# Optimization experiments

Measured on AMD Instinct MI355X. Metric: run time of the kernel, lower is better.

Reference implementation:

```python
import jax, jax.numpy as jnp
from jax import lax
import numpy as np

BIG_I = jnp.int32(2 ** 30)   # background / +inf sentinel for labels
BIG_F = 1e6                  # +inf sentinel for distances (max true dist ~ H+W)


def cc_labels(fg):
    """8-connected component labeling via iterative min-label propagation.
    fg: (H, W) bool. Returns int32 labels; background pixels get BIG_I.
    Two pixels are in the same component iff their labels are equal
    (labels are min linear index of the component, which is all the loss uses)."""
    H, W = fg.shape
    lab0 = jnp.where(fg, jnp.arange(H * W, dtype=jnp.int32).reshape(H, W), BIG_I)

    def neigh_min(lab):
        p = jnp.pad(lab, 1, constant_values=BIG_I)
        m = lab
        for di in (-1, 0, 1):
            for dj in (-1, 0, 1):
                m = jnp.minimum(m, lax.dynamic_slice(p, (1 + di, 1 + dj), (H, W)))
        return jnp.where(fg, m, BIG_I)

    def body(state):
        lab, _ = state
        new = neigh_min(lab)
        return new, jnp.all(new == lab)

    lab, _ = lax.while_loop(lambda s: ~s[1], body, (lab0, jnp.array(False)))
    return lab


def _dt_axis(d, axis):
    # exact 1D L1 (min-plus, slope 1) lower envelope via forward/backward scans
    d = jnp.moveaxis(d, axis, 0)
    init = jnp.full(d.shape[1:], BIG_F, dtype=d.dtype)
    step = lambda c, x: ((jnp.minimum(x, c + 1.0),) * 2)
    _, fwd = lax.scan(step, init, d)
    _, bwd = lax.scan(step, init, d[::-1])
    return jnp.moveaxis(jnp.minimum(fwd, bwd[::-1]), 0, axis)


def l1_distance_transform(zero_mask):
    """Exact L1 distance to the nearest True pixel of zero_mask
    (== cv2.distanceTransform(DIST_L1, maskSize=3) on a binary image whose
    zero set is zero_mask). L1 DT is separable -> two 1D passes."""
    d0 = jnp.where(zero_mask, 0.0, BIG_F).astype(jnp.float32)
    return _dt_axis(_dt_axis(d0, 0), 1)


def _loss_one(result, pts):
    WEIGHT, GAP_W, CLUST_W = 100.0, 10.0, 90.0
    r0 = result[pts[0, 0], pts[0, 1]]
    r1 = result[pts[1, 0], pts[1, 1]]
    soa_inv = jnp.sum(1.0 - result)  # soa_cells_inv (per-pixel loop in original)
    fallback = (2.0 - (r0 + r1)) * WEIGHT
    loss_start = fallback

    img = lax.stop_gradient(jnp.round(result))  # result.round().detach()
    fg = img > 0.5
    lab = cc_labels(fg)
    sl = lab[pts[0, 0], pts[0, 1]]
    el = lab[pts[1, 0], pts[1, 1]]
    both = fg[pts[0, 0], pts[0, 1]] & fg[pts[1, 0], pts[1, 1]]  # start/end labels != 0

    # start_cluster = pixels of the start component (same set when start==end)
    start_mask = fg & (lab == sl) & both
    # modified label image: end component -> 0, everything else nonzero
    end_zero = fg & (lab == el)
    dist = l1_distance_transform(end_zero)  # distance to end component
    min_d = jnp.minimum(dist[pts[0, 0], pts[0, 1]],
                        jnp.min(jnp.where(start_mask, dist, BIG_F)))

    gap_loss = jnp.where(both, min_d * soa_inv * GAP_W * soa_inv, fallback)
    cluster_cells = jnp.sum(jnp.where(start_mask, result, 0.0))
    cluster_pen = jnp.where(both, cluster_cells * CLUST_W, fallback)
    return loss_start, gap_loss, cluster_pen


def setup_inputs():
    key = jax.random.key(0)
    k1, k2 = jax.random.split(key)
    result_given = jax.random.uniform(k1, (4, 1, 512, 512), dtype=jnp.float32)
    points_given = jax.random.randint(k2, (4, 2, 2), 0, 512, dtype=jnp.int32)
    return {"result_given": result_given, "points_given": points_given}


def reference(result_given, points_given):
    # Original loop overwrites loss/gap_loss/cluster_size_penalty each batch
    # iteration -> returned tuple reflects only the last batch element.
    ls, gl, cp = jax.vmap(_loss_one)(result_given[:, 0], points_given)
    return ls[-1], gl[-1], cp[-1]
```

## Files before the change

kernel.cpp:

```cpp
#include <hip/hip_runtime.h>

#define H 512
#define W 512
#define NPIX (H * W)
#define BIG_I 1073741824
#define BIG_F 1.0e6f
#define INF30 1.0e30f

struct Scal {
  float soa;
  unsigned int min_bits;
  float cluster;
  int sl;
  int pad[4];
};

__device__ unsigned g_bar1, g_bar2, g_bar3, g_doneS, g_doneD;

__device__ __forceinline__ void gbar(unsigned* cnt, bool wait) {
  __syncthreads();
  if (threadIdx.x == 0) {
    __threadfence();
    unsigned old = atomicAdd(cnt, 1u);
    if (wait) {
      unsigned target = (old & ~255u) + 256u;
      while (__hip_atomic_load(cnt, __ATOMIC_RELAXED, __HIP_MEMORY_SCOPE_AGENT) < target)
        __builtin_amdgcn_s_sleep(1);
      __threadfence();
    }
  }
  __syncthreads();
}

__device__ __forceinline__ int rep(int* lab, int v) {
  int cur = lab[v];
  if (cur == v) return v;
  int prev = v, next;
  while (cur > (next = lab[cur])) { lab[prev] = next; prev = cur; cur = next; }
  return cur;
}
__device__ __forceinline__ void unite(int* lab, int a, int b) {
  int ra = rep(lab, a), rb = rep(lab, b);
  while (ra != rb) {
    if (ra < rb) { int t = ra; ra = rb; rb = t; }
    int old = atomicCAS(&lab[ra], ra, rb);
    if (old == ra) break;
    ra = rep(lab, old);
    rb = rep(lab, rb);
  }
}
__device__ __forceinline__ int root_ph(int* lab, int v) {
  int p = lab[v];
  if (p == v) return v;
  int gp = lab[p];
  while (p != gp) {
    lab[v] = gp;
    v = p; p = gp; gp = lab[p];
  }
  return p;
}
__device__ __forceinline__ int runstart(unsigned m, int c) {
  unsigned z = ~m & ((1u << c) - 1u);
  return z ? (32 - __clz((int)z)) : 0;
}

__global__ __launch_bounds__(256) void k_fused(
    const float* __restrict__ img, const int* __restrict__ pts,
    int* __restrict__ lab, int* __restrict__ lab2, float* __restrict__ dist,
    Scal* __restrict__ s, float* __restrict__ Asoa, float* __restrict__ out) {
  __shared__ union {
    struct { int uf[1024]; unsigned rmask[32]; float red[4]; } p1;
    struct { float laf[32][8]; float lbb[32][8]; float smin[4]; } p4;
  } sh;
  __shared__ int sflag;

  const int t = threadIdx.x;
  const int b = blockIdx.x;

  const int tileX = (b & 15) * 32;
  const int tileY = (b >> 4) * 32;
  const int r = t >> 3, c0 = (t & 7) * 4;
  const float4 x4 = *(const float4*)(img + (tileY + r) * W + tileX + c0);

  const int p0 = pts[0] * W + pts[1];
  const int p1x = pts[2] * W + pts[3];
  const float r0 = img[p0], r1 = img[p1x];
  const bool both = (rintf(r0) > 0.5f) && (rintf(r1) > 0.5f);
  const float fb = (2.0f - (r0 + r1)) * 100.0f;
  if (!both) {
    if (b == 0 && t == 0) { out[0] = fb; out[1] = fb; out[2] = fb; }
    return;
  }
  if (b == 0 && t == 0) {
    s->min_bits = __float_as_uint(BIG_F);
    s->cluster = 0.0f;
  }

  {
    float acc = 4.0f - (x4.x + x4.y + x4.z + x4.w);
    unsigned nib = (rintf(x4.x) > 0.5f ? 1u : 0u) | (rintf(x4.y) > 0.5f ? 2u : 0u)
                 | (rintf(x4.z) > 0.5f ? 4u : 0u) | (rintf(x4.w) > 0.5f ? 8u : 0u);
    unsigned m = nib << c0;
    m |= __shfl_xor(m, 1, 64);
    m |= __shfl_xor(m, 2, 64);
    m |= __shfl_xor(m, 4, 64);
    if ((t & 7) == 0) sh.p1.rmask[r] = m;
    unsigned startM = m & ~(m << 1);
    #pragma unroll
    for (int k = 0; k < 4; ++k) {
      int c = c0 + k;
      if ((startM >> c) & 1u) sh.p1.uf[(r << 5) + c] = (r << 5) + c;
    }
    __syncthreads();
    if (r > 0) {
      unsigned ma = sh.p1.rmask[r - 1];
      unsigned upM = m & ma & (~(m << 1) | ~(ma << 1));
      unsigned dL  = startM & (ma << 1) & ~ma;
      unsigned dR  = (m & ~(m >> 1)) & (ma >> 1) & ~ma;
      #pragma unroll
      for (int k = 0; k < 4; ++k) {
        int c = c0 + k;
        int myS = (r << 5) + runstart(m, c);
        if ((upM >> c) & 1u) unite(sh.p1.uf, myS, ((r - 1) << 5) + runstart(ma, c));
        if ((dL  >> c) & 1u) unite(sh.p1.uf, myS, ((r - 1) << 5) + runstart(ma, c - 1));
        if ((dR  >> c) & 1u) unite(sh.p1.uf, myS, ((r - 1) << 5) + c + 1);
      }
    }
    __syncthreads();
    int o[4];
    #pragma unroll
    for (int k = 0; k < 4; ++k) {
      int c = c0 + k;
      if ((m >> c) & 1u) {
        int rt = rep(sh.p1.uf, (r << 5) + runstart(m, c));
        o[k] = (tileY + (rt >> 5)) * W + tileX + (rt & 31);
      } else o[k] = BIG_I;
    }
    *(int4*)(lab + (tileY + r) * W + tileX + c0) = make_int4(o[0], o[1], o[2], o[3]);
    for (int off = 32; off; off >>= 1) acc += __shfl_down(acc, off, 64);
    if ((t & 63) == 0) sh.p1.red[t >> 6] = acc;
    __syncthreads();
    if (t == 0) Asoa[b] = sh.p1.red[0] + sh.p1.red[1] + sh.p1.red[2] + sh.p1.red[3];
  }
  gbar(&g_bar1, true);

  {
    int lane = t & 63;
    int gid = b * 256 + t;
    if (gid < 7680) {
      int bb = gid >> 9, j = gid & 511;
      int i = (bb + 1) * 32;
      int p = i * W + j, q = p - W;
      int a  = lab[p];
      int u0 = lab[q];
      int um = (j > 0)   ? lab[q - 1] : BIG_I;
      int up = (j < 511) ? lab[q + 1] : BIG_I;
      int a_prev = __shfl_up(a, 1, 64);
      if (lane == 0) a_prev = (j > 0) ? lab[p - 1] : BIG_I;
      if (a != BIG_I) {
        if (um != BIG_I && a != a_prev) unite(lab, a, um);
        if (u0 != BIG_I && u0 != um) unite(lab, a, u0);
        if (up != BIG_I && up != u0 && !(u0 == BIG_I && up == um)) unite(lab, a, up);
      }
    } else if (gid < 15360) {
      int t2 = gid - 7680;
      int bb = t2 >> 9, i = t2 & 511;
      int j = (bb + 1) * 32;
      int p = i * W + j;
      int lp = lab[p], ll = lab[p - 1];
      int lpp = __shfl_up(lp, 1, 64);
      int llp = __shfl_up(ll, 1, 64);
      if (lane == 0) {
        lpp = (i > 0) ? lab[p - W] : BIG_I;
        llp = (i > 0) ? lab[p - W - 1] : BIG_I;
      }
      bool fgp = lp != BIG_I, fgl = ll != BIG_I;
      if (fgp && fgl && !(lp == lpp && ll == llp)) unite(lab, lp, ll);
      if ((i & 31) && i > 0) {
        if (fgp && llp != BIG_I && lp != lpp) unite(lab, lp, llp);
        if (fgl && lpp != BIG_I && ll != llp) unite(lab, ll, lpp);
      }
    } else if (b == 60 && t < 64) {
      float a = Asoa[t] + Asoa[t + 64] + Asoa[t + 128] + Asoa[t + 192];
      for (int off = 32; off; off >>= 1) a += __shfl_down(a, off, 64);
      if (t == 0) s->soa = a;
    }
  }
  gbar(&g_bar2, true);

  if (t < 128) {
    int lane = t & 63;
    int row = b * 2 + (t >> 6);
    int el = -1, sl2 = -1;
    if (lane == 0) {
      el = root_ph(lab, lab[p1x]);
      sl2 = root_ph(lab, lab[p0]);
      if (t == 0) sflag = (el == sl2);
      if (b == 0 && t == 0) s->sl = sl2;
    }
    el = __shfl(el, 0, 64);
    sl2 = __shfl(sl2, 0, 64);
    const bool skip = (el == sl2);
    const int4* lp = (const int4*)(lab + row * W) + lane * 2;
    int4 a = lp[0], bq = lp[1];
    int v[8] = {a.x, a.y, a.z, a.w, bq.x, bq.y, bq.z, bq.w};
    int psrc = -1, proot = -1;
    #pragma unroll
    for (int k = 0; k < 8; ++k) {
      if (v[k] == BIG_I) continue;
      if (v[k] == psrc) { v[k] = proot; continue; }
      psrc = v[k];
      proot = root_ph(lab, v[k]);
      v[k] = proot;
    }
    if (!skip) {
      int4* l2 = (int4*)(lab2 + row * W) + lane * 2;
      l2[0] = make_int4(v[0], v[1], v[2], v[3]);
      l2[1] = make_int4(v[4], v[5], v[6], v[7]);
    }
    const float4* ip = (const float4*)(img + row * W) + lane * 2;
    float4 i0q = ip[0], i1q = ip[1];
    float cv = 0.0f;
    if (v[0] == sl2) cv += i0q.x;
    if (v[1] == sl2) cv += i0q.y;
    if (v[2] == sl2) cv += i0q.z;
    if (v[3] == sl2) cv += i0q.w;
    if (v[4] == sl2) cv += i1q.x;
    if (v[5] == sl2) cv += i1q.y;
    if (v[6] == sl2) cv += i1q.z;
    if (v[7] == sl2) cv += i1q.w;
    for (int off = 32; off; off >>= 1) cv += __shfl_down(cv, off, 64);
    if (lane == 0 && cv != 0.0f) atomicAdd(&s->cluster, cv);
    if (!skip) {
      float d[8];
      #pragma unroll
      for (int k = 0; k < 8; ++k) d[k] = (v[k] == el) ? 0.0f : BIG_F;
      int j0 = lane * 8;
      float pf[8], sb[8];
      float m = INF30;
      #pragma unroll
      for (int k = 0; k < 8; ++k) { m = fminf(m, d[k] - (float)(j0 + k)); pf[k] = m; }
      float tf = m;
      m = INF30;
      #pragma unroll
      for (int k = 7; k >= 0; --k) { m = fminf(m, d[k] + (float)(j0 + k)); sb[k] = m; }
      float tb = m;
      float vv = tf;
      #pragma unroll
      for (int off = 1; off < 64; off <<= 1) {
        float u = __shfl_up(vv, off, 64);
        if (lane >= off) vv = fminf(vv, u);
      }
      float ef = __shfl_up(vv, 1, 64); if (lane == 0) ef = INF30;
      vv = tb;
      #pragma unroll
      for (int off = 1; off < 64; off <<= 1) {
        float u = __shfl_down(vv, off, 64);
        if (lane < 64 - off) vv = fminf(vv, u);
      }
      float eb = __shfl_down(vv, 1, 64); if (lane == 63) eb = INF30;
      float o[8];
      #pragma unroll
      for (int k = 0; k < 8; ++k) {
        float j = (float)(j0 + k);
        o[k] = fminf(j + fminf(ef, pf[k]), -j + fminf(eb, sb[k]));
      }
      float4* dp = (float4*)(dist + row * W) + lane * 2;
      dp[0] = make_float4(o[0], o[1], o[2], o[3]);
      dp[1] = make_float4(o[4], o[5], o[6], o[7]);
    }
  }
  __syncthreads();
  const bool skipb = sflag != 0;

  if (skipb) {
    if (t == 0) {
      __threadfence();
      unsigned old = atomicAdd(&g_doneS, 1u);
      if ((old & 255u) == 255u) {
        out[0] = fb;
        out[1] = 0.0f;
        float cl = atomicAdd(&s->cluster, 0.0f);
        out[2] = cl * 90.0f;
      }
    }
    return;
  }

  if (b >= 64) { gbar(&g_bar3, false); return; }
  gbar(&g_bar3, true);

  {
    int sg = t >> 3, c = t & 7;
    int j = b * 8 + c;
    int i0 = sg * 16;
    float rr[16];
    float fa = INF30, fbk = INF30;
    #pragma unroll
    for (int il = 0; il < 16; ++il) {
      rr[il] = dist[(i0 + il) * W + j];
      float fi = (float)(i0 + il);
      fa = fminf(fa, rr[il] - fi);
      fbk = fminf(fbk, rr[il] + fi);
    }
    sh.p4.laf[sg][c] = fa;
    sh.p4.lbb[sg][c] = fbk;
    __syncthreads();
    float cf = INF30, cb = INF30;
    #pragma unroll
    for (int bb = 0; bb < 32; ++bb) {
      if (bb < sg) cf = fminf(cf, sh.p4.laf[bb][c]);
      if (bb > sg) cb = fminf(cb, sh.p4.lbb[bb][c]);
    }
    int slv = s->sl;
    float ff[16];
    float m = cf;
    #pragma unroll
    for (int il = 0; il < 16; ++il) {
      float fi = (float)(i0 + il);
      m = fminf(m, rr[il] - fi);
      ff[il] = fi + m;
    }
    m = cb;
    float dv = BIG_F;
    #pragma unroll
    for (int il = 15; il >= 0; --il) {
      int pix = (i0 + il) * W + j;
      float fi = (float)(i0 + il);
      m = fminf(m, rr[il] + fi);
      float o = fminf(ff[il], m - fi);
      if (lab2[pix] == slv) dv = fminf(dv, o);
      if (pix == p0) dv = fminf(dv, o);
    }
    for (int off = 32; off; off >>= 1)
      dv = fminf(dv, __shfl_down(dv, off, 64));
    if ((t & 63) == 0) sh.p4.smin[t >> 6] = dv;
    __syncthreads();
    if (t == 0) {
      float mm = fminf(fminf(sh.p4.smin[0], sh.p4.smin[1]),
                       fminf(sh.p4.smin[2], sh.p4.smin[3]));
      atomicMin(&s->min_bits, __float_as_uint(mm));
      __threadfence();
      unsigned old = atomicAdd(&g_doneD, 1u);
      if ((old & 63u) == 63u) {
        out[0] = fb;
        float min_d = __uint_as_float(atomicOr(&s->min_bits, 0u));
        float cl = atomicAdd(&s->cluster, 0.0f);
        float soa = s->soa;
        out[1] = min_d * soa * 10.0f * soa;
        out[2] = cl * 90.0f;
      }
    }
  }
}

extern "C" void kernel_launch(void* const* d_in, const int* in_sizes, int n_in,
                              void* d_out, int out_size, void* d_ws, size_t ws_size,
                              hipStream_t stream) {
  const float* img = (const float*)d_in[0] + 3 * NPIX;
  const int* pts = (const int*)d_in[1] + 3 * 4;
  float* out = (float*)d_out;

  int* lab = (int*)d_ws;
  float* dist = (float*)d_ws + NPIX;
  char* base = (char*)d_ws + (size_t)2 * NPIX * 4;
  Scal* s = (Scal*)base;
  float* Asoa = (float*)(base + 64);
  int* lab2 = (int*)(base + 64 + 1024);

  k_fused<<<256, 256, 0, stream>>>(img, pts, lab, lab2, dist, s, Asoa, out);
}
```

Before: 55.33 us.

## Replace global barrier before tile merge with neighbor flag waits

Each block now publishes a per-tile epoch flag and waits only for its adjacent tiles before merging its own boundary edges, instead of a grid-wide barrier followed by a grid-strided merge. Label finalization and cluster accumulation move into the tile's own registers, reusing the already-loaded pixels, and a separate barrier is added before the row distance pass, which now reads the finalized labels. The intent is to cut global barrier latency and redundant loads. In exchange it adds an epoch ticket, boundary-compressing find with relaxed atomics, and one more grid barrier on the non-skip path.

```diff
diff --git a/kernel.cpp b/kernel.cpp
--- a/kernel.cpp
+++ b/kernel.cpp
@@ -11,11 +11,12 @@
   float soa;
   unsigned int min_bits;
   float cluster;
-  int sl;
-  int pad[4];
+  int pad[5];
 };
 
-__device__ unsigned g_bar1, g_bar2, g_bar3, g_doneS, g_doneD;
+__device__ unsigned g_ticket;
+__device__ unsigned g_tileflag[256];
+__device__ unsigned g_barM, g_barR, g_barC, g_doneS, g_doneD;
 
 __device__ __forceinline__ void gbar(unsigned* cnt, bool wait) {
   __syncthreads();
@@ -59,6 +60,26 @@
   }
   return p;
 }
+__device__ __forceinline__ int lda(int* p) {
+  return __hip_atomic_load(p, __ATOMIC_RELAXED, __HIP_MEMORY_SCOPE_AGENT);
+}
+__device__ __forceinline__ int rep_bp(int* lab, int v) {
+  int cur = lda(&lab[v]);
+  if (cur == v) return v;
+  int prev = v, next;
+  while (cur > (next = lda(&lab[cur]))) { lab[prev] = next; prev = cur; cur = next; }
+  return cur;
+}
+__device__ __forceinline__ void unite_bp(int* lab, int a, int b) {
+  int ra = rep_bp(lab, a), rb = rep_bp(lab, b);
+  while (ra != rb) {
+    if (ra < rb) { int t = ra; ra = rb; rb = t; }
+    int old = atomicCAS(&lab[ra], ra, rb);
+    if (old == ra) break;
+    ra = rep_bp(lab, old);
+    rb = rep_bp(lab, rb);
+  }
+}
 __device__ __forceinline__ int runstart(unsigned m, int c) {
   unsigned z = ~m & ((1u << c) - 1u);
   return z ? (32 - __clz((int)z)) : 0;
@@ -72,13 +93,13 @@
     struct { int uf[1024]; unsigned rmask[32]; float red[4]; } p1;
     struct { float laf[32][8]; float lbb[32][8]; float smin[4]; } p4;
   } sh;
-  __shared__ int sflag;
+  __shared__ int s_sl, s_el, s_skip;
+  __shared__ float cred[4];
 
   const int t = threadIdx.x;
   const int b = blockIdx.x;
-
-  const int tileX = (b & 15) * 32;
-  const int tileY = (b >> 4) * 32;
+  const int tY = b >> 4, tX = b & 15;
+  const int tileX = tX * 32, tileY = tY * 32;
   const int r = t >> 3, c0 = (t & 7) * 4;
   const float4 x4 = *(const float4*)(img + (tileY + r) * W + tileX + c0);
 
@@ -91,11 +112,19 @@
     if (b == 0 && t == 0) { out[0] = fb; out[1] = fb; out[2] = fb; }
     return;
   }
+  unsigned ep1 = 0;
+  if (t < 64) {
+    unsigned tk = 0;
+    if (t == 0) tk = atomicAdd(&g_ticket, 1u);
+    tk = __shfl(tk, 0, 64);
+    ep1 = (tk >> 8) + 1u;
+  }
   if (b == 0 && t == 0) {
     s->min_bits = __float_as_uint(BIG_F);
     s->cluster = 0.0f;
   }
 
+  int o[4];
   {
     float acc = 4.0f - (x4.x + x4.y + x4.z + x4.w);
     unsigned nib = (rintf(x4.x) > 0.5f ? 1u : 0u) | (rintf(x4.y) > 0.5f ? 2u : 0u)
@@ -127,7 +156,6 @@
       }
     }
     __syncthreads();
-    int o[4];
     #pragma unroll
     for (int k = 0; k < 4; ++k) {
       int c = c0 + k;
@@ -140,144 +168,115 @@
     for (int off = 32; off; off >>= 1) acc += __shfl_down(acc, off, 64);
     if ((t & 63) == 0) sh.p1.red[t >> 6] = acc;
     __syncthreads();
-    if (t == 0) Asoa[b] = sh.p1.red[0] + sh.p1.red[1] + sh.p1.red[2] + sh.p1.red[3];
-  }
-  gbar(&g_bar1, true);
-
+    if (t == 0) {
+      Asoa[b] = sh.p1.red[0] + sh.p1.red[1] + sh.p1.red[2] + sh.p1.red[3];
+      __threadfence();
+      __hip_atomic_store(&g_tileflag[b], ep1, __ATOMIC_RELAXED,
+                         __HIP_MEMORY_SCOPE_AGENT);
+    }
+  }
+
+  if (t < 64) {
+    const bool hasH = tY < 15, hasV = tX < 15;
+    int nb = -1;
+    if (t == 0 && hasH)            nb = b + 16;
+    if (t == 1 && hasH && tX > 0)  nb = b + 15;
+    if (t == 2 && hasH && tX > 0)  nb = b - 1;
+    if (t == 3 && hasV)            nb = b + 1;
+    if (t == 4 && hasV && tY > 0)  nb = b - 16;
+    if (t == 5 && hasV && tY > 0)  nb = b - 15;
+    if (nb >= 0) {
+      while (__hip_atomic_load(&g_tileflag[nb], __ATOMIC_RELAXED,
+                               __HIP_MEMORY_SCOPE_AGENT) < ep1)
+        __builtin_amdgcn_s_sleep(1);
+    }
+    __threadfence();
+    if (t < 32) {
+      if (hasH) {
+        const int j = tileX + t;
+        const int p = (tileY + 32) * W + j, q = p - W;
+        int a  = lab[p];
+        int u0 = lab[q];
+        int um = (j > 0)   ? lab[q - 1] : BIG_I;
+        int up = (j < 511) ? lab[q + 1] : BIG_I;
+        int a_prev = __shfl_up(a, 1, 64);
+        if (t == 0) a_prev = (j > 0) ? lab[p - 1] : BIG_I;
+        if (a != BIG_I) {
+          if (um != BIG_I && a != a_prev) unite_bp(lab, a, um);
+          if (u0 != BIG_I && u0 != um) unite_bp(lab, a, u0);
+          if (up != BIG_I && up != u0 && !(u0 == BIG_I && up == um)) unite_bp(lab, a, up);
+        }
+      }
+    } else {
+      if (hasV) {
+        const int il = t - 32;
+        const int i = tileY + il;
+        const int p = i * W + tileX + 32;
+        int lp = lab[p], ll = lab[p - 1];
+        int lpp = __shfl_up(lp, 1, 64);
+        int llp = __shfl_up(ll, 1, 64);
+        if (il == 0) {
+          lpp = (i > 0) ? lab[p - W] : BIG_I;
+          llp = (i > 0) ? lab[p - W - 1] : BIG_I;
+        }
+        bool fgp = lp != BIG_I, fgl = ll != BIG_I;
+        if (fgp && fgl && !(lp == lpp && ll == llp)) unite_bp(lab, lp, ll);
+        if (il != 0) {
+          if (fgp && llp != BIG_I && lp != lpp) unite_bp(lab, lp, llp);
+          if (fgl && lpp != BIG_I && ll != llp) unite_bp(lab, ll, lpp);
+        }
+      }
+    }
+  }
+  gbar(&g_barM, true);
+
+  if (t == 0) {
+    int e  = root_ph(lab, lab[p1x]);
+    int s2 = root_ph(lab, lab[p0]);
+    s_el = e; s_sl = s2; s_skip = (e == s2);
+  }
+  if (b == 60 && t >= 64 && t < 128) {
+    int l = t & 63;
+    float a = Asoa[l] + Asoa[l + 64] + Asoa[l + 128] + Asoa[l + 192];
+    for (int off = 32; off; off >>= 1) a += __shfl_down(a, off, 64);
+    if (l == 0) s->soa = a;
+  }
+  int fin[4];
   {
-    int lane = t & 63;
-    int gid = b * 256 + t;
-    if (gid < 7680) {
-      int bb = gid >> 9, j = gid & 511;
-      int i = (bb + 1) * 32;
-      int p = i * W + j, q = p - W;
-      int a  = lab[p];
-      int u0 = lab[q];
-      int um = (j > 0)   ? lab[q - 1] : BIG_I;
-      int up = (j < 511) ? lab[q + 1] : BIG_I;
-      int a_prev = __shfl_up(a, 1, 64);
-      if (lane == 0) a_prev = (j > 0) ? lab[p - 1] : BIG_I;
-      if (a != BIG_I) {
-        if (um != BIG_I && a != a_prev) unite(lab, a, um);
-        if (u0 != BIG_I && u0 != um) unite(lab, a, u0);
-        if (up != BIG_I && up != u0 && !(u0 == BIG_I && up == um)) unite(lab, a, up);
-      }
-    } else if (gid < 15360) {
-      int t2 = gid - 7680;
-      int bb = t2 >> 9, i = t2 & 511;
-      int j = (bb + 1) * 32;
-      int p = i * W + j;
-      int lp = lab[p], ll = lab[p - 1];
-      int lpp = __shfl_up(lp, 1, 64);
-      int llp = __shfl_up(ll, 1, 64);
-      if (lane == 0) {
-        lpp = (i > 0) ? lab[p - W] : BIG_I;
-        llp = (i > 0) ? lab[p - W - 1] : BIG_I;
-      }
-      bool fgp = lp != BIG_I, fgl = ll != BIG_I;
-      if (fgp && fgl && !(lp == lpp && ll == llp)) unite(lab, lp, ll);
-      if ((i & 31) && i > 0) {
-        if (fgp && llp != BIG_I && lp != lpp) unite(lab, lp, llp);
-        if (fgl && lpp != BIG_I && ll != llp) unite(lab, ll, lpp);
-      }
-    } else if (b == 60 && t < 64) {
-      float a = Asoa[t] + Asoa[t + 64] + Asoa[t + 128] + Asoa[t + 192];
-      for (int off = 32; off; off >>= 1) a += __shfl_down(a, off, 64);
-      if (t == 0) s->soa = a;
-    }
-  }
-  gbar(&g_bar2, true);
-
-  if (t < 128) {
-    int lane = t & 63;
-    int row = b * 2 + (t >> 6);
-    int el = -1, sl2 = -1;
-    if (lane == 0) {
-      el = root_ph(lab, lab[p1x]);
-      sl2 = root_ph(lab, lab[p0]);
-      if (t == 0) sflag = (el == sl2);
-      if (b == 0 && t == 0) s->sl = sl2;
-    }
-    el = __shfl(el, 0, 64);
-    sl2 = __shfl(sl2, 0, 64);
-    const bool skip = (el == sl2);
-    const int4* lp = (const int4*)(lab + row * W) + lane * 2;
-    int4 a = lp[0], bq = lp[1];
-    int v[8] = {a.x, a.y, a.z, a.w, bq.x, bq.y, bq.z, bq.w};
     int psrc = -1, proot = -1;
     #pragma unroll
-    for (int k = 0; k < 8; ++k) {
-      if (v[k] == BIG_I) continue;
-      if (v[k] == psrc) { v[k] = proot; continue; }
-      psrc = v[k];
-      proot = root_ph(lab, v[k]);
-      v[k] = proot;
-    }
-    if (!skip) {
-      int4* l2 = (int4*)(lab2 + row * W) + lane * 2;
-      l2[0] = make_int4(v[0], v[1], v[2], v[3]);
-      l2[1] = make_int4(v[4], v[5], v[6], v[7]);
-    }
-    const float4* ip = (const float4*)(img + row * W) + lane * 2;
-    float4 i0q = ip[0], i1q = ip[1];
-    float cv = 0.0f;
-    if (v[0] == sl2) cv += i0q.x;
-    if (v[1] == sl2) cv += i0q.y;
-    if (v[2] == sl2) cv += i0q.z;
-    if (v[3] == sl2) cv += i0q.w;
-    if (v[4] == sl2) cv += i1q.x;
-    if (v[5] == sl2) cv += i1q.y;
-    if (v[6] == sl2) cv += i1q.z;
-    if (v[7] == sl2) cv += i1q.w;
-    for (int off = 32; off; off >>= 1) cv += __shfl_down(cv, off, 64);
-    if (lane == 0 && cv != 0.0f) atomicAdd(&s->cluster, cv);
-    if (!skip) {
-      float d[8];
-      #pragma unroll
-      for (int k = 0; k < 8; ++k) d[k] = (v[k] == el) ? 0.0f : BIG_F;
-      int j0 = lane * 8;
-      float pf[8], sb[8];
-      float m = INF30;
-      #pragma unroll
-      for (int k = 0; k < 8; ++k) { m = fminf(m, d[k] - (float)(j0 + k)); pf[k] = m; }
-      float tf = m;
-      m = INF30;
-      #pragma unroll
-      for (int k = 7; k >= 0; --k) { m = fminf(m, d[k] + (float)(j0 + k)); sb[k] = m; }
-      float tb = m;
-      float vv = tf;
-      #pragma unroll
-      for (int off = 1; off < 64; off <<= 1) {
-        float u = __shfl_up(vv, off, 64);
-        if (lane >= off) vv = fminf(vv, u);
-      }
-      float ef = __shfl_up(vv, 1, 64); if (lane == 0) ef = INF30;
-      vv = tb;
-      #pragma unroll
-      for (int off = 1; off < 64; off <<= 1) {
-        float u = __shfl_down(vv, off, 64);
-        if (lane < 64 - off) vv = fminf(vv, u);
-      }
-      float eb = __shfl_down(vv, 1, 64); if (lane == 63) eb = INF30;
-      float o[8];
-      #pragma unroll
-      for (int k = 0; k < 8; ++k) {
-        float j = (float)(j0 + k);
-        o[k] = fminf(j + fminf(ef, pf[k]), -j + fminf(eb, sb[k]));
-      }
-      float4* dp = (float4*)(dist + row * W) + lane * 2;
-      dp[0] = make_float4(o[0], o[1], o[2], o[3]);
-      dp[1] = make_float4(o[4], o[5], o[6], o[7]);
+    for (int k = 0; k < 4; ++k) {
+      if (o[k] == BIG_I) { fin[k] = BIG_I; continue; }
+      if (o[k] == psrc) { fin[k] = proot; continue; }
+      psrc = o[k];
+      proot = root_ph(lab, o[k]);
+      fin[k] = proot;
     }
   }
   __syncthreads();
-  const bool skipb = sflag != 0;
-
-  if (skipb) {
+  const int slv = s_sl, elv = s_el;
+  const bool skip = s_skip != 0;
+  float cv = 0.0f;
+  if (fin[0] == slv) cv += x4.x;
+  if (fin[1] == slv) cv += x4.y;
+  if (fin[2] == slv) cv += x4.z;
+  if (fin[3] == slv) cv += x4.w;
+  for (int off = 32; off; off >>= 1) cv += __shfl_down(cv, off, 64);
+  if ((t & 63) == 0) cred[t >> 6] = cv;
+  __syncthreads();
+  if (t == 0) {
+    float tot = cred[0] + cred[1] + cred[2] + cred[3];
+    if (tot != 0.0f) atomicAdd(&s->cluster, tot);
+  }
+  if (!skip)
+    *(int4*)(lab2 + (tileY + r) * W + tileX + c0) = make_int4(fin[0], fin[1], fin[2], fin[3]);
+
+  if (skip) {
     if (t == 0) {
       __threadfence();
       unsigned old = atomicAdd(&g_doneS, 1u);
       if ((old & 255u) == 255u) {
+        __threadfence();
         out[0] = fb;
         out[1] = 0.0f;
         float cl = atomicAdd(&s->cluster, 0.0f);
@@ -287,8 +286,52 @@
     return;
   }
 
-  if (b >= 64) { gbar(&g_bar3, false); return; }
-  gbar(&g_bar3, true);
+  gbar(&g_barR, true);
+  if (t < 128) {
+    int lane = t & 63;
+    int row = b * 2 + (t >> 6);
+    const int4* lp2 = (const int4*)(lab2 + row * W) + lane * 2;
+    int4 a = lp2[0], bq = lp2[1];
+    int v[8] = {a.x, a.y, a.z, a.w, bq.x, bq.y, bq.z, bq.w};
+    float d[8];
+    #pragma unroll
+    for (int k = 0; k < 8; ++k) d[k] = (v[k] == elv) ? 0.0f : BIG_F;
+    int j0 = lane * 8;
+    float pf[8], sb[8];
+    float m = INF30;
+    #pragma unroll
+    for (int k = 0; k < 8; ++k) { m = fminf(m, d[k] - (float)(j0 + k)); pf[k] = m; }
+    float tf = m;
+    m = INF30;
+    #pragma unroll
+    for (int k = 7; k >= 0; --k) { m = fminf(m, d[k] + (float)(j0 + k)); sb[k] = m; }
+    float tb = m;
+    float vv = tf;
+    #pragma unroll
+    for (int off = 1; off < 64; off <<= 1) {
+      float u = __shfl_up(vv, off, 64);
+      if (lane >= off) vv = fminf(vv, u);
+    }
+    float ef = __shfl_up(vv, 1, 64); if (lane == 0) ef = INF30;
+    vv = tb;
+    #pragma unroll
+    for (int off = 1; off < 64; off <<= 1) {
+      float u = __shfl_down(vv, off, 64);
+      if (lane < 64 - off) vv = fminf(vv, u);
+    }
+    float eb = __shfl_down(vv, 1, 64); if (lane == 63) eb = INF30;
+    float oo[8];
+    #pragma unroll
+    for (int k = 0; k < 8; ++k) {
+      float j = (float)(j0 + k);
+      oo[k] = fminf(j + fminf(ef, pf[k]), -j + fminf(eb, sb[k]));
+    }
+    float4* dp = (float4*)(dist + row * W) + lane * 2;
+    dp[0] = make_float4(oo[0], oo[1], oo[2], oo[3]);
+    dp[1] = make_float4(oo[4], oo[5], oo[6], oo[7]);
+  }
+  if (b >= 64) { gbar(&g_barC, false); return; }
+  gbar(&g_barC, true);
 
   {
     int sg = t >> 3, c = t & 7;
@@ -312,7 +355,6 @@
       if (bb < sg) cf = fminf(cf, sh.p4.laf[bb][c]);
       if (bb > sg) cb = fminf(cb, sh.p4.lbb[bb][c]);
     }
-    int slv = s->sl;
     float ff[16];
     float m = cf;
     #pragma unroll
@@ -328,9 +370,9 @@
       int pix = (i0 + il) * W + j;
       float fi = (float)(i0 + il);
       m = fminf(m, rr[il] + fi);
-      float o = fminf(ff[il], m - fi);
-      if (lab2[pix] == slv) dv = fminf(dv, o);
-      if (pix == p0) dv = fminf(dv, o);
+      float oo = fminf(ff[il], m - fi);
+      if (lab2[pix] == slv) dv = fminf(dv, oo);
+      if (pix == p0) dv = fminf(dv, oo);
     }
     for (int off = 32; off; off >>= 1)
       dv = fminf(dv, __shfl_down(dv, off, 64));
@@ -343,6 +385,7 @@
       __threadfence();
       unsigned old = atomicAdd(&g_doneD, 1u);
       if ((old & 63u) == 63u) {
+        __threadfence();
         out[0] = fb;
         float min_d = __uint_as_float(atomicOr(&s->min_bits, 0u));
         float cl = atomicAdd(&s->cluster, 0.0f);
```

Result: no change. 54.64 us (median of 2 runs) (-1.2%).
